# Performance work log

Measured on AMD Instinct MI355X. Metric: run time of the kernel, lower is better.

## Reference

```python
import jax, jax.numpy as jnp
import numpy as np

N_NODES = 100000
N_EDGES = 1600000
N_GRAPHS = 64
IN_DIM, HID_DIM, OUT_DIM = 128, 256, 256


def setup_inputs() -> dict:
    key = jax.random.key(0)
    ks = jax.random.split(key, 7)
    x = jax.random.normal(ks[0], (N_NODES, IN_DIM), dtype=jnp.float32)
    edge_index = jax.random.randint(ks[1], (2, N_EDGES), 0, N_NODES, dtype=jnp.int32)
    batch = jnp.sort(jax.random.randint(ks[2], (N_NODES,), 0, N_GRAPHS, dtype=jnp.int32))
    # Glorot-style init for GCN linear weights, zero bias (as in PyG defaults)
    W1 = jax.random.normal(ks[3], (IN_DIM, HID_DIM), dtype=jnp.float32) / np.sqrt(IN_DIM)
    b1 = jnp.zeros((HID_DIM,), dtype=jnp.float32)
    W2 = jax.random.normal(ks[4], (HID_DIM, OUT_DIM), dtype=jnp.float32) / np.sqrt(HID_DIM)
    b2 = jnp.zeros((OUT_DIM,), dtype=jnp.float32)
    return {"x": x, "edge_index": edge_index, "batch": batch,
            "W1": W1, "b1": b1, "W2": W2, "b2": b2}


def reference(x, edge_index, batch, W1, b1, W2, b2):
    N = x.shape[0]
    # --- GCN normalization with self-loops (computed once, edge structure fixed) ---
    loops = jnp.arange(N, dtype=edge_index.dtype)
    row = jnp.concatenate([edge_index[0], loops])  # source nodes  [E+N]
    col = jnp.concatenate([edge_index[1], loops])  # target nodes  [E+N]
    deg = jax.ops.segment_sum(jnp.ones_like(col, dtype=x.dtype), col, num_segments=N)
    dinv = jax.lax.rsqrt(jnp.maximum(deg, 1.0))    # deg >= 1 due to self-loops
    norm = dinv[row] * dinv[col]                   # [E+N]

    def gcn_conv(h, W, b):
        h = h @ W                                  # linear transform first (PyG order)
        msg = h[row] * norm[:, None]               # gather + normalize  [E+N, D]
        agg = jax.ops.segment_sum(msg, col, num_segments=N)  # scatter-add
        return agg + b

    h = jax.nn.relu(gcn_conv(x, W1, b1))
    h = jax.nn.relu(gcn_conv(h, W2, b2))

    # --- global mean pool over graph ids ---
    s = jax.ops.segment_sum(h, batch, num_segments=N_GRAPHS)           # [G, D]
    cnt = jax.ops.segment_sum(jnp.ones((N, 1), h.dtype), batch, num_segments=N_GRAPHS)
    return s / jnp.maximum(cnt, 1.0)
```

## Files before the change

kernel.cpp:

```cpp
#include <hip/hip_runtime.h>

typedef __attribute__((ext_vector_type(8))) short short8;
typedef __attribute__((ext_vector_type(4))) float float4v;
typedef __attribute__((ext_vector_type(4))) uint uint4v;

#define CAP 64
#define NREP 8
#define CAPR 16

__device__ __forceinline__ ushort f2bf(float f) {
    uint u = __float_as_uint(f);
    u += 0x7fffu + ((u >> 16) & 1u);
    return (ushort)(u >> 16);
}
__device__ __forceinline__ float bf2f(ushort h) {
    return __uint_as_float((uint)h << 16);
}
__device__ __forceinline__ void acc8(float* acc, uint4 v) {
    acc[0] += __uint_as_float(v.x << 16);
    acc[1] += __uint_as_float(v.x & 0xffff0000u);
    acc[2] += __uint_as_float(v.y << 16);
    acc[3] += __uint_as_float(v.y & 0xffff0000u);
    acc[4] += __uint_as_float(v.z << 16);
    acc[5] += __uint_as_float(v.z & 0xffff0000u);
    acc[6] += __uint_as_float(v.w << 16);
    acc[7] += __uint_as_float(v.w & 0xffff0000u);
}
__device__ __forceinline__ int clampi(int v, int n) {
    return (int)min((uint)v, (uint)(n - 1));
}

__global__ void countW_k(const int* __restrict__ col, int* __restrict__ cnt,
                         unsigned char* __restrict__ rank, int E, int N, int ebl,
                         const float* __restrict__ W1, ushort* __restrict__ W1p,
                         const float* __restrict__ W2, ushort* __restrict__ W2p) {
    int b = blockIdx.x;
    if (b < ebl) {
        int e = b * 256 + threadIdx.x;
        int r = b & (NREP - 1);
        if (e < E) {
            int c = col[e];
            int p = atomicAdd(&cnt[(size_t)r * N + c], 1);
            rank[e] = (unsigned char)min(p, 255);
        }
    } else {
        int idx = (b - ebl) * 256 + threadIdx.x;
        if (idx < 32768) {
            int j = idx & 7, lane = (idx >> 3) & 63;
            int s = (idx >> 9) % 4, nt = (idx >> 9) / 4;
            int k = 32 * s + (lane >> 4) * 8 + j;
            int c = nt * 16 + (lane & 15);
            W1p[idx] = f2bf(W1[k * 256 + c]);
        } else if (idx < 32768 + 65536) {
            int q = idx - 32768;
            int j = q & 7, lane = (q >> 3) & 63;
            int s = (q >> 9) % 8, nt = (q >> 9) / 8;
            int k = 32 * s + (lane >> 4) * 8 + j;
            int c = nt * 16 + (lane & 15);
            W2p[q] = f2bf(W2[k * 256 + c]);
        }
    }
}

__global__ void scan_k(const int* __restrict__ cnt, int* __restrict__ idg,
                       unsigned long long* __restrict__ cnt8, int N) {
    int v = blockIdx.x * 256 + threadIdx.x;
    if (v >= N) return;
    int deg = 0;
    unsigned long long pk = 0;
#pragma unroll
    for (int r = 0; r < NREP; ++r) {
        int c = cnt[(size_t)r * N + v];
        pk |= (unsigned long long)min(c, 255) << (8 * r);
        deg += c;
    }
    idg[v] = deg;
    cnt8[v] = pk;
}

__global__ void placeS_k(const int* __restrict__ row, const int* __restrict__ col,
                         const unsigned char* __restrict__ rank,
                         int* __restrict__ staging, int E, int N, int ebl,
                         const float* __restrict__ x, const int* __restrict__ idg,
                         ushort* __restrict__ xb, int n4) {
    int b = blockIdx.x;
    if (b < ebl) {
        int e = b * 256 + threadIdx.x;
        int r = b & (NREP - 1);
        if (e < E) {
            int c = col[e];
            int rk = rank[e];
            if (rk < CAPR)
                staging[((size_t)r * N + c) * CAPR + rk] = row[e];
        }
    } else {
        int i = (b - ebl) * 256 + threadIdx.x;
        if (i < n4) {
            int node = i >> 5;
            float di = rsqrtf((float)(idg[node] + 1));
            float4 v = ((const float4*)x)[i];
            ushort4 o;
            o.x = f2bf(v.x * di); o.y = f2bf(v.y * di);
            o.z = f2bf(v.z * di); o.w = f2bf(v.w * di);
            ((ushort4*)xb)[i] = o;
        }
    }
}

__global__ __launch_bounds__(256) void compact_k(const int* __restrict__ staging,
                                                 const unsigned long long* __restrict__ cnt8,
                                                 int* __restrict__ eidx, int N) {
    int t = threadIdx.x;
    int node = blockIdx.x * 32 + (t >> 3);
    if (node >= N) return;
    int r = t & 7;
    unsigned long long pk = cnt8[node];
    int base = 0, m = 0;
#pragma unroll
    for (int rr = 0; rr < 8; ++rr) {
        int mv = min((int)((pk >> (8 * rr)) & 255ULL), CAPR);
        if (rr < r) base += mv;
        if (rr == r) m = mv;
    }
    const int* sp = staging + ((size_t)r * N + node) * CAPR;
    int* op = eidx + (size_t)node * CAP;
    for (int k = 0; k < m; ++k) {
        int pos = base + k;
        if (pos < CAP) op[pos] = sp[k];
    }
}

__global__ __launch_bounds__(256) void agg128_k(const ushort* __restrict__ g,
                                                ushort* __restrict__ out,
                                                const int* __restrict__ idg,
                                                const int* __restrict__ eidx, int n) {
    int w = threadIdx.x >> 6, lane = threadIdx.x & 63;
    int q = lane >> 4, sub = lane & 15;
    int i = blockIdx.x * 16 + w * 4 + q;
    if (i >= n) return;
    const ushort* gp = g + (size_t)sub * 8;
    float acc[8] = {};
    {
        uint4 v = *(const uint4*)(gp + (size_t)i * 128);
        acc8(acc, v);
    }
    int deg = idg[i];
    int cnt = min(deg, CAP);
    const int* ep = eidx + (size_t)i * CAP;
    int j = 0;
    for (; j + 8 <= cnt; j += 8) {
        int s0 = clampi(__builtin_nontemporal_load(ep + j), n);
        int s1 = clampi(__builtin_nontemporal_load(ep + j + 1), n);
        int s2 = clampi(__builtin_nontemporal_load(ep + j + 2), n);
        int s3 = clampi(__builtin_nontemporal_load(ep + j + 3), n);
        int s4 = clampi(__builtin_nontemporal_load(ep + j + 4), n);
        int s5 = clampi(__builtin_nontemporal_load(ep + j + 5), n);
        int s6 = clampi(__builtin_nontemporal_load(ep + j + 6), n);
        int s7 = clampi(__builtin_nontemporal_load(ep + j + 7), n);
        uint4 v0 = *(const uint4*)(gp + (size_t)s0 * 128);
        uint4 v1 = *(const uint4*)(gp + (size_t)s1 * 128);
        uint4 v2 = *(const uint4*)(gp + (size_t)s2 * 128);
        uint4 v3 = *(const uint4*)(gp + (size_t)s3 * 128);
        uint4 v4 = *(const uint4*)(gp + (size_t)s4 * 128);
        uint4 v5 = *(const uint4*)(gp + (size_t)s5 * 128);
        uint4 v6 = *(const uint4*)(gp + (size_t)s6 * 128);
        uint4 v7 = *(const uint4*)(gp + (size_t)s7 * 128);
        acc8(acc, v0); acc8(acc, v1); acc8(acc, v2); acc8(acc, v3);
        acc8(acc, v4); acc8(acc, v5); acc8(acc, v6); acc8(acc, v7);
    }
    if (j + 4 <= cnt) {
        int s0 = clampi(__builtin_nontemporal_load(ep + j), n);
        int s1 = clampi(__builtin_nontemporal_load(ep + j + 1), n);
        int s2 = clampi(__builtin_nontemporal_load(ep + j + 2), n);
        int s3 = clampi(__builtin_nontemporal_load(ep + j + 3), n);
        uint4 v0 = *(const uint4*)(gp + (size_t)s0 * 128);
        uint4 v1 = *(const uint4*)(gp + (size_t)s1 * 128);
        uint4 v2 = *(const uint4*)(gp + (size_t)s2 * 128);
        uint4 v3 = *(const uint4*)(gp + (size_t)s3 * 128);
        acc8(acc, v0); acc8(acc, v1); acc8(acc, v2); acc8(acc, v3);
        j += 4;
    }
    if (j + 2 <= cnt) {
        int s0 = clampi(__builtin_nontemporal_load(ep + j), n);
        int s1 = clampi(__builtin_nontemporal_load(ep + j + 1), n);
        uint4 v0 = *(const uint4*)(gp + (size_t)s0 * 128);
        uint4 v1 = *(const uint4*)(gp + (size_t)s1 * 128);
        acc8(acc, v0); acc8(acc, v1);
        j += 2;
    }
    if (j < cnt) {
        int s0 = clampi(__builtin_nontemporal_load(ep + j), n);
        uint4 v0 = *(const uint4*)(gp + (size_t)s0 * 128);
        acc8(acc, v0);
    }
    float di = rsqrtf((float)(deg + 1));
    uint4v o;
    o.x = (uint)f2bf(acc[0] * di) | ((uint)f2bf(acc[1] * di) << 16);
    o.y = (uint)f2bf(acc[2] * di) | ((uint)f2bf(acc[3] * di) << 16);
    o.z = (uint)f2bf(acc[4] * di) | ((uint)f2bf(acc[5] * di) << 16);
    o.w = (uint)f2bf(acc[6] * di) | ((uint)f2bf(acc[7] * di) << 16);
    __builtin_nontemporal_store(o, (uint4v*)(out + (size_t)i * 128 + sub * 8));
}

__global__ __launch_bounds__(256) void agg256_k(const ushort* __restrict__ g,
                                                ushort* __restrict__ out,
                                                const int* __restrict__ idg,
                                                const int* __restrict__ eidx, int n) {
    int w = threadIdx.x >> 6, lane = threadIdx.x & 63;
    int half = lane >> 5, sub = lane & 31;
    int i = blockIdx.x * 8 + w * 2 + half;
    if (i >= n) return;
    const ushort* gp = g + (size_t)sub * 8;
    float acc[8] = {};
    {
        uint4 v = *(const uint4*)(gp + (size_t)i * 256);
        acc8(acc, v);
    }
    int deg = idg[i];
    int cnt = min(deg, CAP);
    const int* ep = eidx + (size_t)i * CAP;
    int j = 0;
    for (; j + 8 <= cnt; j += 8) {
        int s0 = clampi(__builtin_nontemporal_load(ep + j), n);
        int s1 = clampi(__builtin_nontemporal_load(ep + j + 1), n);
        int s2 = clampi(__builtin_nontemporal_load(ep + j + 2), n);
        int s3 = clampi(__builtin_nontemporal_load(ep + j + 3), n);
        int s4 = clampi(__builtin_nontemporal_load(ep + j + 4), n);
        int s5 = clampi(__builtin_nontemporal_load(ep + j + 5), n);
        int s6 = clampi(__builtin_nontemporal_load(ep + j + 6), n);
        int s7 = clampi(__builtin_nontemporal_load(ep + j + 7), n);
        uint4 v0 = *(const uint4*)(gp + (size_t)s0 * 256);
        uint4 v1 = *(const uint4*)(gp + (size_t)s1 * 256);
        uint4 v2 = *(const uint4*)(gp + (size_t)s2 * 256);
        uint4 v3 = *(const uint4*)(gp + (size_t)s3 * 256);
        uint4 v4 = *(const uint4*)(gp + (size_t)s4 * 256);
        uint4 v5 = *(const uint4*)(gp + (size_t)s5 * 256);
        uint4 v6 = *(const uint4*)(gp + (size_t)s6 * 256);
        uint4 v7 = *(const uint4*)(gp + (size_t)s7 * 256);
        acc8(acc, v0); acc8(acc, v1); acc8(acc, v2); acc8(acc, v3);
        acc8(acc, v4); acc8(acc, v5); acc8(acc, v6); acc8(acc, v7);
    }
    if (j + 4 <= cnt) {
        int s0 = clampi(__builtin_nontemporal_load(ep + j), n);
        int s1 = clampi(__builtin_nontemporal_load(ep + j + 1), n);
        int s2 = clampi(__builtin_nontemporal_load(ep + j + 2), n);
        int s3 = clampi(__builtin_nontemporal_load(ep + j + 3), n);
        uint4 v0 = *(const uint4*)(gp + (size_t)s0 * 256);
        uint4 v1 = *(const uint4*)(gp + (size_t)s1 * 256);
        uint4 v2 = *(const uint4*)(gp + (size_t)s2 * 256);
        uint4 v3 = *(const uint4*)(gp + (size_t)s3 * 256);
        acc8(acc, v0); acc8(acc, v1); acc8(acc, v2); acc8(acc, v3);
        j += 4;
    }
    if (j + 2 <= cnt) {
        int s0 = clampi(__builtin_nontemporal_load(ep + j), n);
        int s1 = clampi(__builtin_nontemporal_load(ep + j + 1), n);
        uint4 v0 = *(const uint4*)(gp + (size_t)s0 * 256);
        uint4 v1 = *(const uint4*)(gp + (size_t)s1 * 256);
        acc8(acc, v0); acc8(acc, v1);
        j += 2;
    }
    if (j < cnt) {
        int s0 = clampi(__builtin_nontemporal_load(ep + j), n);
        uint4 v0 = *(const uint4*)(gp + (size_t)s0 * 256);
        acc8(acc, v0);
    }
    float di = rsqrtf((float)(deg + 1));
    uint4v o;
    o.x = (uint)f2bf(acc[0] * di) | ((uint)f2bf(acc[1] * di) << 16);
    o.y = (uint)f2bf(acc[2] * di) | ((uint)f2bf(acc[3] * di) << 16);
    o.z = (uint)f2bf(acc[4] * di) | ((uint)f2bf(acc[5] * di) << 16);
    o.w = (uint)f2bf(acc[6] * di) | ((uint)f2bf(acc[7] * di) << 16);
    __builtin_nontemporal_store(o, (uint4v*)(out + (size_t)i * 256 + sub * 8));
}

template <int K, bool SCALE>
__global__ __launch_bounds__(512) void gemm_ldsw_k(const ushort* __restrict__ A,
                                                   const ushort* __restrict__ Wp,
                                                   const float* __restrict__ bias,
                                                   const int* __restrict__ idg,
                                                   ushort* __restrict__ C, int M) {
    constexpr int S = K / 32;
    constexpr int STAGE_US = 4 * S * 64 * 8;
    __shared__ ushort ldsW[STAGE_US];
    int tid = threadIdx.x, wv = tid >> 6, lane = tid & 63;
    int quad = lane >> 4, l15 = lane & 15;
    int rowBase = blockIdx.x * 128 + wv * 16;
    int arow = rowBase + l15; if (arow > M - 1) arow = M - 1;
    const ushort* abase = A + (size_t)arow * K + quad * 8;
    short8 af[S];
#pragma unroll
    for (int s = 0; s < S; ++s) af[s] = *(const short8*)(abase + 32 * s);

    float diRow[4];
    if (SCALE) {
#pragma unroll
        for (int r = 0; r < 4; ++r) {
            int rr = min(rowBase + quad * 4 + r, M - 1);
            diRow[r] = rsqrtf((float)(idg[rr] + 1));
        }
    }

#pragma unroll
    for (int st = 0; st < 4; ++st) {
        __syncthreads();
        {
            const uint4* src = (const uint4*)(Wp + (size_t)st * STAGE_US);
            uint4* dst = (uint4*)ldsW;
#pragma unroll
            for (int it = 0; it < STAGE_US / 8 / 512; ++it)
                dst[it * 512 + tid] = src[it * 512 + tid];
        }
        __syncthreads();
        float4v acc[4];
#pragma unroll
        for (int nt = 0; nt < 4; ++nt) {
            float4v a = {0.f, 0.f, 0.f, 0.f};
#pragma unroll
            for (int s = 0; s < S; ++s) {
                short8 bf = *(const short8*)&ldsW[((nt * S + s) * 64 + lane) * 8];
                a = __builtin_amdgcn_mfma_f32_16x16x32_bf16(af[s], bf, a, 0, 0, 0);
            }
            acc[nt] = a;
        }
#pragma unroll
        for (int nt = 0; nt < 4; ++nt) {
            int col = (st * 4 + nt) * 16 + l15;
            float b = bias[col];
#pragma unroll
            for (int r = 0; r < 4; ++r) {
                int rw = rowBase + quad * 4 + r;
                if (rw < M) {
                    float v = fmaxf(acc[nt][r] + b, 0.f);
                    if (SCALE) v *= diRow[r];
                    C[(size_t)rw * 256 + col] = f2bf(v);
                }
            }
        }
    }
}

__global__ __launch_bounds__(512) void gemm_pool_k(const ushort* __restrict__ A,
                                                   const ushort* __restrict__ Wp,
                                                   const float* __restrict__ bias,
                                                   const int* __restrict__ batch,
                                                   float* __restrict__ psum,
                                                   float* __restrict__ spill, int M) {
    constexpr int S = 8;
    constexpr int STAGE_US = 4 * S * 64 * 8;
    __shared__ ushort ldsW[STAGE_US];
    __shared__ float ldsSum[4][256];
    int tid = threadIdx.x, wv = tid >> 6, lane = tid & 63;
    int quad = lane >> 4, l15 = lane & 15;
    int rowBase = blockIdx.x * 128 + wv * 16;
    int arow = rowBase + l15; if (arow > M - 1) arow = M - 1;
    const ushort* abase = A + (size_t)arow * 256 + quad * 8;
    short8 af[S];
#pragma unroll
    for (int s = 0; s < S; ++s) af[s] = *(const short8*)(abase + 32 * s);

    int b0 = batch[blockIdx.x * 128];
    int sg[4];
#pragma unroll
    for (int r = 0; r < 4; ++r) {
        int rw = rowBase + quad * 4 + r;
        sg[r] = (rw < M) ? (batch[rw] - b0) : -1;
    }
    bool tFast = (sg[0] == sg[1]) && (sg[1] == sg[2]) && (sg[2] == sg[3]) &&
                 sg[0] >= 0 && sg[0] < 4;
    int sw = __builtin_amdgcn_readfirstlane(sg[0]);
    bool waveFast = __all(tFast && (sg[0] == sw));

    for (int z = tid; z < 1024; z += 512) ((float*)ldsSum)[z] = 0.f;

#pragma unroll
    for (int st = 0; st < 4; ++st) {
        __syncthreads();
        {
            const uint4* src = (const uint4*)(Wp + (size_t)st * STAGE_US);
            uint4* dst = (uint4*)ldsW;
#pragma unroll
            for (int it = 0; it < STAGE_US / 8 / 512; ++it)
                dst[it * 512 + tid] = src[it * 512 + tid];
        }
        __syncthreads();
        float4v acc[4];
#pragma unroll
        for (int nt = 0; nt < 4; ++nt) {
            float4v a = {0.f, 0.f, 0.f, 0.f};
#pragma unroll
            for (int s = 0; s < S; ++s) {
                short8 bf = *(const short8*)&ldsW[((nt * S + s) * 64 + lane) * 8];
                a = __builtin_amdgcn_mfma_f32_16x16x32_bf16(af[s], bf, a, 0, 0, 0);
            }
            acc[nt] = a;
        }
#pragma unroll
        for (int nt = 0; nt < 4; ++nt) {
            int col = (st * 4 + nt) * 16 + l15;
            float b = bias[col];
            if (waveFast) {
                float v = fmaxf(acc[nt][0] + b, 0.f) + fmaxf(acc[nt][1] + b, 0.f)
                        + fmaxf(acc[nt][2] + b, 0.f) + fmaxf(acc[nt][3] + b, 0.f);
                v += __shfl_xor(v, 16);
                v += __shfl_xor(v, 32);
                if (quad == 0) atomicAdd(&ldsSum[sw][col], v);
            } else {
#pragma unroll
                for (int r = 0; r < 4; ++r) {
                    if (sg[r] >= 0) {
                        float v = fmaxf(acc[nt][r] + b, 0.f);
                        if (sg[r] < 4) atomicAdd(&ldsSum[sg[r]][col], v);
                        else atomicAdd(&spill[(b0 + sg[r]) * 256 + col], v);
                    }
                }
            }
        }
    }
    __syncthreads();
    for (int z = tid; z < 1024; z += 512)
        psum[(size_t)blockIdx.x * 1024 + z] = ((float*)ldsSum)[z];
}

__global__ void final2_k(float* __restrict__ out, const float* __restrict__ psum,
                         const float* __restrict__ spill,
                         const int* __restrict__ batch, int n) {
    __shared__ int sSE[2];
    int g = blockIdx.x, d = threadIdx.x;
    if (d == 0) {
        int lo = 0, hi = n;
        while (lo < hi) { int mid = (lo + hi) >> 1; if (batch[mid] < g) lo = mid + 1; else hi = mid; }
        sSE[0] = lo;
        lo = 0; hi = n; int g1 = g + 1;
        while (lo < hi) { int mid = (lo + hi) >> 1; if (batch[mid] < g1) lo = mid + 1; else hi = mid; }
        sSE[1] = lo;
    }
    __syncthreads();
    int s = sSE[0], e = sSE[1];
    float sum = spill[g * 256 + d];
    if (e > s) {
        int bA = s >> 7, bB = (e - 1) >> 7;
        for (int b = bA; b <= bB; ++b) {
            int seg = g - batch[b * 128];
            if (seg >= 0 && seg < 4)
                sum += psum[((size_t)b * 4 + seg) * 256 + d];
        }
    }
    out[g * 256 + d] = sum / fmaxf((float)(e - s), 1.f);
}

extern "C" void kernel_launch(void* const* d_in, const int* in_sizes, int n_in,
                              void* d_out, int out_size, void* d_ws, size_t ws_size,
                              hipStream_t stream) {
    const float* x  = (const float*)d_in[0];
    const int*   ei = (const int*)d_in[1];
    const int*   batch = (const int*)d_in[2];
    const float* W1 = (const float*)d_in[3];
    const float* b1 = (const float*)d_in[4];
    const float* W2 = (const float*)d_in[5];
    const float* b2 = (const float*)d_in[6];
    float* out = (float*)d_out;

    const int N  = in_sizes[2];
    const int E  = in_sizes[1] / 2;
    const int* row = ei;
    const int* col = ei + E;

    char* p = (char*)d_ws;
    auto alloc = [&](size_t bytes) {
        char* q = p;
        p += (bytes + 255) & ~(size_t)255;
        return q;
    };
    int*    idg    = (int*)alloc((size_t)N * 4);
    int*    eidx   = (int*)alloc((size_t)N * CAP * 4);
    ushort* W1p    = (ushort*)alloc(16 * 4 * 64 * 8 * 2);
    ushort* W2p    = (ushort*)alloc(16 * 8 * 64 * 8 * 2);
    ushort* xb     = (ushort*)alloc((size_t)N * 128 * 2);
    ushort* aggX   = (ushort*)alloc((size_t)N * 128 * 2);
    ushort* g1     = (ushort*)alloc((size_t)N * 256 * 2);
    ushort* aggH   = (ushort*)alloc((size_t)N * 256 * 2);
    int*    cnt    = (int*)alloc((size_t)NREP * N * 4);
    float*  spill  = (float*)alloc(64 * 256 * 4);
    unsigned char* rank = (unsigned char*)alloc((size_t)E);
    unsigned long long* cnt8 = (unsigned long long*)alloc((size_t)N * 8);
    int*    staging = (int*)alloc((size_t)NREP * N * CAPR * 4);
    const int gb2 = (N + 127) / 128;
    float*  psum   = (float*)alloc((size_t)gb2 * 4 * 256 * 4);

    const int nb  = (N + 255) / 256;
    const int ebl = (E + 255) / 256;
    const int n4  = N * 32;
    const int cvtb = (n4 + 255) / 256;
    const int wpb  = 98304 / 256;

    hipMemsetAsync(cnt, 0, (size_t)NREP * N * 4 + 64 * 256 * 4, stream);

    countW_k<<<ebl + wpb, 256, 0, stream>>>(col, cnt, rank, E, N, ebl,
                                            W1, W1p, W2, W2p);
    scan_k<<<nb, 256, 0, stream>>>(cnt, idg, cnt8, N);
    placeS_k<<<ebl + cvtb, 256, 0, stream>>>(row, col, rank, staging, E, N, ebl,
                                             x, idg, xb, n4);
    compact_k<<<(N + 31) / 32, 256, 0, stream>>>(staging, cnt8, eidx, N);

    agg128_k<<<(N + 15) / 16, 256, 0, stream>>>(xb, aggX, idg, eidx, N);
    gemm_ldsw_k<128, true><<<gb2, 512, 0, stream>>>(aggX, W1p, b1, idg, g1, N);

    agg256_k<<<(N + 7) / 8, 256, 0, stream>>>(g1, aggH, idg, eidx, N);
    gemm_pool_k<<<gb2, 512, 0, stream>>>(aggH, W2p, b2, batch, psum, spill, N);

    final2_k<<<64, 256, 0, stream>>>(out, psum, spill, batch, N);
}
```

Baseline: 477.1 us.

## Fuse edge-list compaction into first aggregation kernel via shared memory

Removes the separate compact_k launch: agg128_k now gathers each node's source indices from the per-replica staging buffers into shared memory, uses them directly for the layer-1 gather, and also writes the compacted eidx for reuse by agg256_k. Edge counts now come from the packed cnt8 fill counts instead of the in-degree. This drops one kernel launch and one round-trip of the index array through global memory, at the cost of extra work and uncoalesced staging reads inside the aggregation kernel. There is no barrier between the shared-memory writes and reads, which relies on the writing and reading lanes sharing a wavefront.

```diff
diff --git a/kernel.cpp b/kernel.cpp
--- a/kernel.cpp
+++ b/kernel.cpp
@@ -28,6 +28,12 @@
 }
 __device__ __forceinline__ int clampi(int v, int n) {
     return (int)min((uint)v, (uint)(n - 1));
+}
+__device__ __forceinline__ int fillcnt(unsigned long long pk) {
+    int c = 0;
+#pragma unroll
+    for (int r = 0; r < 8; ++r) c += min((int)((pk >> (8 * r)) & 255ULL), CAPR);
+    return min(c, CAP);
 }
 
 __global__ void countW_k(const int* __restrict__ col, int* __restrict__ cnt,
@@ -107,37 +113,37 @@
     }
 }
 
-__global__ __launch_bounds__(256) void compact_k(const int* __restrict__ staging,
-                                                 const unsigned long long* __restrict__ cnt8,
-                                                 int* __restrict__ eidx, int N) {
-    int t = threadIdx.x;
-    int node = blockIdx.x * 32 + (t >> 3);
-    if (node >= N) return;
-    int r = t & 7;
-    unsigned long long pk = cnt8[node];
-    int base = 0, m = 0;
-#pragma unroll
-    for (int rr = 0; rr < 8; ++rr) {
-        int mv = min((int)((pk >> (8 * rr)) & 255ULL), CAPR);
-        if (rr < r) base += mv;
-        if (rr == r) m = mv;
-    }
-    const int* sp = staging + ((size_t)r * N + node) * CAPR;
-    int* op = eidx + (size_t)node * CAP;
-    for (int k = 0; k < m; ++k) {
-        int pos = base + k;
-        if (pos < CAP) op[pos] = sp[k];
-    }
-}
-
 __global__ __launch_bounds__(256) void agg128_k(const ushort* __restrict__ g,
                                                 ushort* __restrict__ out,
                                                 const int* __restrict__ idg,
-                                                const int* __restrict__ eidx, int n) {
+                                                const unsigned long long* __restrict__ cnt8,
+                                                const int* __restrict__ staging,
+                                                int* __restrict__ eidx, int n) {
+    __shared__ int idxL[16][CAP];
     int w = threadIdx.x >> 6, lane = threadIdx.x & 63;
     int q = lane >> 4, sub = lane & 15;
-    int i = blockIdx.x * 16 + w * 4 + q;
+    int nl = w * 4 + q;
+    int i = blockIdx.x * 16 + nl;
     if (i >= n) return;
+
+    unsigned long long pk = cnt8[i];
+    int base = 0;
+#pragma unroll
+    for (int r = 0; r < NREP; ++r) {
+        int m = min((int)((pk >> (8 * r)) & 255ULL), CAPR);
+        if (sub < m) {
+            int pos = base + sub;
+            if (pos < CAP) {
+                int v = staging[((size_t)r * n + i) * CAPR + sub];
+                idxL[nl][pos] = v;
+                eidx[(size_t)i * CAP + pos] = v;
+            }
+        }
+        base += m;
+    }
+    int cnt = min(base, CAP);
+    const int* ep = idxL[nl];
+
     const ushort* gp = g + (size_t)sub * 8;
     float acc[8] = {};
     {
@@ -145,18 +151,12 @@
         acc8(acc, v);
     }
     int deg = idg[i];
-    int cnt = min(deg, CAP);
-    const int* ep = eidx + (size_t)i * CAP;
     int j = 0;
     for (; j + 8 <= cnt; j += 8) {
-        int s0 = clampi(__builtin_nontemporal_load(ep + j), n);
-        int s1 = clampi(__builtin_nontemporal_load(ep + j + 1), n);
-        int s2 = clampi(__builtin_nontemporal_load(ep + j + 2), n);
-        int s3 = clampi(__builtin_nontemporal_load(ep + j + 3), n);
-        int s4 = clampi(__builtin_nontemporal_load(ep + j + 4), n);
-        int s5 = clampi(__builtin_nontemporal_load(ep + j + 5), n);
-        int s6 = clampi(__builtin_nontemporal_load(ep + j + 6), n);
-        int s7 = clampi(__builtin_nontemporal_load(ep + j + 7), n);
+        int s0 = clampi(ep[j], n),     s1 = clampi(ep[j + 1], n);
+        int s2 = clampi(ep[j + 2], n), s3 = clampi(ep[j + 3], n);
+        int s4 = clampi(ep[j + 4], n), s5 = clampi(ep[j + 5], n);
+        int s6 = clampi(ep[j + 6], n), s7 = clampi(ep[j + 7], n);
         uint4 v0 = *(const uint4*)(gp + (size_t)s0 * 128);
         uint4 v1 = *(const uint4*)(gp + (size_t)s1 * 128);
         uint4 v2 = *(const uint4*)(gp + (size_t)s2 * 128);
@@ -169,10 +169,8 @@
         acc8(acc, v4); acc8(acc, v5); acc8(acc, v6); acc8(acc, v7);
     }
     if (j + 4 <= cnt) {
-        int s0 = clampi(__builtin_nontemporal_load(ep + j), n);
-        int s1 = clampi(__builtin_nontemporal_load(ep + j + 1), n);
-        int s2 = clampi(__builtin_nontemporal_load(ep + j + 2), n);
-        int s3 = clampi(__builtin_nontemporal_load(ep + j + 3), n);
+        int s0 = clampi(ep[j], n),     s1 = clampi(ep[j + 1], n);
+        int s2 = clampi(ep[j + 2], n), s3 = clampi(ep[j + 3], n);
         uint4 v0 = *(const uint4*)(gp + (size_t)s0 * 128);
         uint4 v1 = *(const uint4*)(gp + (size_t)s1 * 128);
         uint4 v2 = *(const uint4*)(gp + (size_t)s2 * 128);
@@ -181,15 +179,14 @@
         j += 4;
     }
     if (j + 2 <= cnt) {
-        int s0 = clampi(__builtin_nontemporal_load(ep + j), n);
-        int s1 = clampi(__builtin_nontemporal_load(ep + j + 1), n);
+        int s0 = clampi(ep[j], n), s1 = clampi(ep[j + 1], n);
         uint4 v0 = *(const uint4*)(gp + (size_t)s0 * 128);
         uint4 v1 = *(const uint4*)(gp + (size_t)s1 * 128);
         acc8(acc, v0); acc8(acc, v1);
         j += 2;
     }
     if (j < cnt) {
-        int s0 = clampi(__builtin_nontemporal_load(ep + j), n);
+        int s0 = clampi(ep[j], n);
         uint4 v0 = *(const uint4*)(gp + (size_t)s0 * 128);
         acc8(acc, v0);
     }
@@ -205,6 +202,7 @@
 __global__ __launch_bounds__(256) void agg256_k(const ushort* __restrict__ g,
                                                 ushort* __restrict__ out,
                                                 const int* __restrict__ idg,
+                                                const unsigned long long* __restrict__ cnt8,
                                                 const int* __restrict__ eidx, int n) {
     int w = threadIdx.x >> 6, lane = threadIdx.x & 63;
     int half = lane >> 5, sub = lane & 31;
@@ -217,7 +215,7 @@
         acc8(acc, v);
     }
     int deg = idg[i];
-    int cnt = min(deg, CAP);
+    int cnt = fillcnt(cnt8[i]);
     const int* ep = eidx + (size_t)i * CAP;
     int j = 0;
     for (; j + 8 <= cnt; j += 8) {
@@ -501,12 +499,11 @@
     scan_k<<<nb, 256, 0, stream>>>(cnt, idg, cnt8, N);
     placeS_k<<<ebl + cvtb, 256, 0, stream>>>(row, col, rank, staging, E, N, ebl,
                                              x, idg, xb, n4);
-    compact_k<<<(N + 31) / 32, 256, 0, stream>>>(staging, cnt8, eidx, N);
-
-    agg128_k<<<(N + 15) / 16, 256, 0, stream>>>(xb, aggX, idg, eidx, N);
+
+    agg128_k<<<(N + 15) / 16, 256, 0, stream>>>(xb, aggX, idg, cnt8, staging, eidx, N);
     gemm_ldsw_k<128, true><<<gb2, 512, 0, stream>>>(aggX, W1p, b1, idg, g1, N);
 
-    agg256_k<<<(N + 7) / 8, 256, 0, stream>>>(g1, aggH, idg, eidx, N);
+    agg256_k<<<(N + 7) / 8, 256, 0, stream>>>(g1, aggH, idg, cnt8, eidx, N);
     gemm_pool_k<<<gb2, 512, 0, stream>>>(aggH, W2p, b2, batch, psum, spill, N);
 
     final2_k<<<64, 256, 0, stream>>>(out, psum, spill, batch, N);
```

Result: faster. 464.9 us (median of 2 runs) (-2.6%).
